# Kernel optimization log

Measured on AMD Instinct MI355X. Metric: run time of the kernel, lower is better.

The kernel has to match this reference:

```python
import jax, jax.numpy as jnp
import numpy as np


def setup_inputs() -> dict:
    key = jax.random.key(0)
    k1, k2, k3, k4 = jax.random.split(key, 4)
    B, T, C, H = 16, 2048, 384, 64
    x = jax.random.normal(k1, (B, T, C), dtype=jnp.float32)
    Wq = jax.random.normal(k2, (C, H), dtype=jnp.float32) * (1.0 / np.sqrt(C))
    Wk = jax.random.normal(k3, (C, H), dtype=jnp.float32) * (1.0 / np.sqrt(C))
    Wv = jax.random.normal(k4, (C, H), dtype=jnp.float32) * (1.0 / np.sqrt(C))
    return {"x": x, "Wq": Wq, "Wk": Wk, "Wv": Wv}


def reference(x, Wq, Wk, Wv):
    # x: [B, T, C]; Wq/Wk/Wv: [C, H]
    T = x.shape[1]
    H = Wk.shape[1]
    q = jnp.einsum('btc,ch->bth', x, Wq)
    k = jnp.einsum('btc,ch->bth', x, Wk)
    v = jnp.einsum('btc,ch->bth', x, Wv)
    scale = 1.0 / jnp.sqrt(jnp.asarray(H, dtype=x.dtype))
    wei = jnp.einsum('bth,bsh->bts', q, k) * scale  # [B, T, T]
    causal = jnp.tril(jnp.ones((T, T), dtype=bool))
    wei = jnp.where(causal, wei, -jnp.inf)
    attn = jax.nn.softmax(wei, axis=-1)
    # dropout p=0 -> identity
    out = jnp.einsum('bts,bsh->bth', attn, v)  # [B, T, H]
    return out
```

## Files before the change

kernel.cpp:

```cpp
#include <hip/hip_runtime.h>
#include <hip/hip_bf16.h>

#define B_ 16
#define T_ 2048
#define C_ 384
#define H_ 64

typedef __attribute__((ext_vector_type(8))) short short8;
typedef __attribute__((ext_vector_type(4))) short short4_t;
typedef __attribute__((ext_vector_type(4))) float floatx4;
typedef __attribute__((ext_vector_type(2))) unsigned int uint2_t;
typedef __attribute__((ext_vector_type(4))) unsigned int uintx4;

#if defined(__has_builtin)
#if __has_builtin(__builtin_amdgcn_mfma_f32_16x16x16bf16_1k)
#define HAVE_MFMA16 1
#endif
#endif

static __device__ __forceinline__ short f2bf(float f) {
    unsigned u = __builtin_bit_cast(unsigned, f);
    u += 0x7FFF + ((u >> 16) & 1);
    return (short)(u >> 16);
}
static __device__ __forceinline__ float bf2f(short s) {
    return __builtin_bit_cast(float, ((unsigned)(unsigned short)s) << 16);
}
static __device__ __forceinline__ unsigned cvt_pk_bf16(float lo, float hi) {
    unsigned r;
    asm("v_cvt_pk_bf16_f32 %0, %1, %2" : "=v"(r) : "v"(lo), "v"(hi));
    return r;
}

__global__ void wt_kernel(const float* __restrict__ Wq, const float* __restrict__ Wk,
                          const float* __restrict__ Wv, short* __restrict__ wt2) {
    int idx = blockIdx.x * 256 + threadIdx.x;
    if (idx >= 12 * 12 * 512) return;
    int f = idx >> 9, within = idx & 511;
    int lane = within >> 3, jj = within & 7;
    int nt16 = f / 12, kc32 = f - nt16 * 12;
    int mat = nt16 >> 2, w = nt16 & 3;
    int quad = lane >> 4, l16 = lane & 15;
    int h = w * 16 + l16;
    int c = kc32 * 32 + quad * 8 + jj;
    const float* W = (mat == 0) ? Wq : ((mat == 1) ? Wk : Wv);
    wt2[idx] = f2bf(W[c * H_ + h]);
}

__global__ __launch_bounds__(256) void qkv_kernel(
        const float* __restrict__ x, const short* __restrict__ wt2,
        short* __restrict__ qo, short* __restrict__ ko, short* __restrict__ vto) {
    __shared__ short xs[32 * 392];

    int b = blockIdx.y, t0 = blockIdx.x * 32;
    int tid = threadIdx.x;

    const float* src = x + (size_t)(b * T_ + t0) * C_;
    for (int i = 0; i < 12; i++) {
        int chunk = i * 256 + tid;
        int row = chunk / 96, off = (chunk % 96) * 4;
        float4 f = *(const float4*)&src[row * 384 + off];
        uint2_t u2;
        u2.x = cvt_pk_bf16(f.x, f.y);
        u2.y = cvt_pk_bf16(f.z, f.w);
        *(uint2_t*)&xs[row * 392 + off] = u2;
    }
    __syncthreads();

    int w = tid >> 6, lane = tid & 63, quad = lane >> 4, l16 = lane & 15;

    floatx4 acc[2][3];
    for (int mt = 0; mt < 2; mt++)
        for (int j = 0; j < 3; j++) acc[mt][j] = (floatx4)0.0f;

    for (int kc = 0; kc < 384; kc += 32) {
        int kc32 = kc >> 5;
        short8 a0 = *(const short8*)&xs[l16 * 392 + kc + quad * 8];
        short8 a1 = *(const short8*)&xs[(16 + l16) * 392 + kc + quad * 8];
        for (int j = 0; j < 3; j++) {
            short8 bf = *(const short8*)&wt2[(((j * 4 + w) * 12) + kc32) * 512 + lane * 8];
            acc[0][j] = __builtin_amdgcn_mfma_f32_16x16x32_bf16(a0, bf, acc[0][j], 0, 0, 0);
            acc[1][j] = __builtin_amdgcn_mfma_f32_16x16x32_bf16(a1, bf, acc[1][j], 0, 0, 0);
        }
    }
    __syncthreads();

    {
        int h = w * 16 + l16;
        for (int j = 0; j < 3; j++)
            for (int mt = 0; mt < 2; mt++)
                for (int r = 0; r < 4; r += 2) {
                    unsigned pk2 = cvt_pk_bf16(acc[mt][j][r], acc[mt][j][r + 1]);
                    int tl0 = mt * 16 + quad * 4 + r;
                    if (j == 0) {
                        xs[tl0 * 72 + h] = (short)pk2;
                        xs[(tl0 + 1) * 72 + h] = (short)(pk2 >> 16);
                    } else if (j == 1) {
                        xs[2304 + tl0 * 72 + h] = (short)pk2;
                        xs[2304 + (tl0 + 1) * 72 + h] = (short)(pk2 >> 16);
                    } else {
                        *(unsigned*)&xs[4608 + h * 40 + tl0] = pk2;
                    }
                }
    }
    __syncthreads();

    {
        int row = tid >> 3, off = (tid & 7) * 8;
        *(short8*)&qo[(size_t)(b * T_ + t0 + row) * H_ + off] = *(const short8*)&xs[row * 72 + off];
        *(short8*)&ko[(size_t)(b * T_ + t0 + row) * H_ + off] = *(const short8*)&xs[2304 + row * 72 + off];
    }
    {
        int h = tid >> 2, off = (tid & 3) * 8;
        *(short8*)&vto[(size_t)(b * H_ + h) * T_ + t0 + off] = *(const short8*)&xs[4608 + h * 40 + off];
    }
}

#define KVSZ (64 * 72)
#define SLOT_BYTES (16384 + 512)

__global__ __launch_bounds__(256) void attn_seg_kernel(
        const short* __restrict__ q, const short* __restrict__ k,
        const short* __restrict__ vt, float* __restrict__ slots) {
    __shared__ short ks[2 * KVSZ];
    __shared__ short vs[2 * KVSZ];
#if !defined(HAVE_MFMA16)
    __shared__ short ps[4 * 16 * 72];
#endif

    int b = blockIdx.y, fid = blockIdx.x, nslot = gridDim.x;
    int tt = 0, cum = 0;
    while (cum + ((2 * tt + 5) >> 2) <= fid) { cum += (2 * tt + 5) >> 2; tt++; }
    int nk = 2 * tt + 2;
    int k0 = (fid - cum) * 4;
    int k1 = min(k0 + 4, nk);

    int tid = threadIdx.x, w = tid >> 6, lane = tid & 63, quad = lane >> 4, l16 = lane & 15;
    int trow0 = tt * 128 + w * 32;

    short8 aq[2][2];
    for (int mt = 0; mt < 2; mt++) {
        const short* qrow = q + (size_t)(b * T_ + trow0 + mt * 16 + l16) * H_;
        aq[mt][0] = *(const short8*)&qrow[quad * 8];
        aq[mt][1] = *(const short8*)&qrow[32 + quad * 8];
    }

    floatx4 o[2][4];
    for (int mt = 0; mt < 2; mt++)
        for (int i = 0; i < 4; i++) o[mt][i] = (floatx4)0.0f;
    float lp[2] = {0.f, 0.f};

    const short* kb0 = k + (size_t)b * T_ * H_;
    const short* vtb = vt + (size_t)b * H_ * T_;

    int srow = tid >> 3, soff = (tid & 7) * 8;
    const float C1 = 0.125f * 1.44269504f;
    const float C2 = 12.0f * 1.44269504f;

    {
        const short* kg = kb0 + (size_t)k0 * 64 * H_;
        const short* vg = vtb + k0 * 64;
        *(short8*)&ks[srow * 72 + soff] = *(const short8*)&kg[srow * H_ + soff];
        *(short8*)&ks[(srow + 32) * 72 + soff] = *(const short8*)&kg[(srow + 32) * H_ + soff];
        *(short8*)&vs[srow * 72 + soff] = *(const short8*)&vg[(size_t)srow * T_ + soff];
        *(short8*)&vs[(srow + 32) * 72 + soff] = *(const short8*)&vg[(size_t)(srow + 32) * T_ + soff];
    }
    __syncthreads();

    int p = 0;
    for (int st = k0; st < k1; st++) {
        bool more = (st + 1 < k1);
        short8 pk0, pk1, pv0, pv1;
        if (more) {
            const short* kg = kb0 + (size_t)(st + 1) * 64 * H_;
            const short* vg = vtb + (st + 1) * 64;
            pk0 = *(const short8*)&kg[srow * H_ + soff];
            pk1 = *(const short8*)&kg[(srow + 32) * H_ + soff];
            pv0 = *(const short8*)&vg[(size_t)srow * T_ + soff];
            pv1 = *(const short8*)&vg[(size_t)(srow + 32) * T_ + soff];
        }
        const short* ksp = ks + p * KVSZ;
        const short* vsp = vs + p * KVSZ;
        int s0 = st * 64;

        floatx4 sacc[2][4];
        for (int mt = 0; mt < 2; mt++)
            for (int nt = 0; nt < 4; nt++) sacc[mt][nt] = (floatx4)0.0f;
        for (int nt = 0; nt < 4; nt++) {
            short8 bk0 = *(const short8*)&ksp[(nt * 16 + l16) * 72 + quad * 8];
            short8 bk1 = *(const short8*)&ksp[(nt * 16 + l16) * 72 + 32 + quad * 8];
            sacc[0][nt] = __builtin_amdgcn_mfma_f32_16x16x32_bf16(bk0, aq[0][0], sacc[0][nt], 0, 0, 0);
            sacc[0][nt] = __builtin_amdgcn_mfma_f32_16x16x32_bf16(bk1, aq[0][1], sacc[0][nt], 0, 0, 0);
            sacc[1][nt] = __builtin_amdgcn_mfma_f32_16x16x32_bf16(bk0, aq[1][0], sacc[1][nt], 0, 0, 0);
            sacc[1][nt] = __builtin_amdgcn_mfma_f32_16x16x32_bf16(bk1, aq[1][1], sacc[1][nt], 0, 0, 0);
        }

        bool diag = (st >= 2 * tt);
#if defined(HAVE_MFMA16)
        short4_t pa[2][4];
        for (int mt = 0; mt < 2; mt++) {
            int q_idx = trow0 + mt * 16 + l16;
            for (int nt = 0; nt < 4; nt++) {
                float pv[4];
                for (int r = 0; r < 4; r++) {
                    float pe = __builtin_amdgcn_exp2f(fmaf(sacc[mt][nt][r], C1, -C2));
                    int s_idx = s0 + nt * 16 + quad * 4 + r;
                    if (diag && (s_idx > q_idx)) pe = 0.0f;
                    lp[mt] += pe;
                    pv[r] = pe;
                }
                uint2_t u;
                u.x = cvt_pk_bf16(pv[0], pv[1]);
                u.y = cvt_pk_bf16(pv[2], pv[3]);
                pa[mt][nt] = __builtin_bit_cast(short4_t, u);
            }
        }
        for (int nh = 0; nh < 4; nh++) {
            const short* vrow = &vsp[(nh * 16 + l16) * 72 + quad * 4];
            for (int c = 0; c < 4; c++) {
                short4_t bv = *(const short4_t*)&vrow[c * 16];
                o[0][nh] = __builtin_amdgcn_mfma_f32_16x16x16bf16_1k(pa[0][c], bv, o[0][nh], 0, 0, 0);
                o[1][nh] = __builtin_amdgcn_mfma_f32_16x16x16bf16_1k(pa[1][c], bv, o[1][nh], 0, 0, 0);
            }
        }
#else
        short* psw = ps + w * 16 * 72;
        short8 ap[2][2];
        for (int mt = 0; mt < 2; mt++) {
            int q_idx = trow0 + mt * 16 + l16;
            for (int nt = 0; nt < 4; nt++)
                for (int r = 0; r < 4; r++) {
                    float pv = __builtin_amdgcn_exp2f(fmaf(sacc[mt][nt][r], C1, -C2));
                    int s_idx = s0 + nt * 16 + quad * 4 + r;
                    if (diag && (s_idx > q_idx)) pv = 0.0f;
                    lp[mt] += pv;
                    psw[l16 * 72 + nt * 16 + quad * 4 + r] = f2bf(pv);
                }
            ap[mt][0] = *(const short8*)&psw[l16 * 72 + quad * 8];
            ap[mt][1] = *(const short8*)&psw[l16 * 72 + 32 + quad * 8];
        }
        for (int nh = 0; nh < 4; nh++) {
            short8 bv0 = *(const short8*)&vsp[(nh * 16 + l16) * 72 + quad * 8];
            short8 bv1 = *(const short8*)&vsp[(nh * 16 + l16) * 72 + 32 + quad * 8];
            o[0][nh] = __builtin_amdgcn_mfma_f32_16x16x32_bf16(ap[0][0], bv0, o[0][nh], 0, 0, 0);
            o[0][nh] = __builtin_amdgcn_mfma_f32_16x16x32_bf16(ap[0][1], bv1, o[0][nh], 0, 0, 0);
            o[1][nh] = __builtin_amdgcn_mfma_f32_16x16x32_bf16(ap[1][0], bv0, o[1][nh], 0, 0, 0);
            o[1][nh] = __builtin_amdgcn_mfma_f32_16x16x32_bf16(ap[1][1], bv1, o[1][nh], 0, 0, 0);
        }
#endif

        if (more) {
            short* kd = ks + (1 - p) * KVSZ;
            short* vd = vs + (1 - p) * KVSZ;
            *(short8*)&kd[srow * 72 + soff] = pk0;
            *(short8*)&kd[(srow + 32) * 72 + soff] = pk1;
            *(short8*)&vd[srow * 72 + soff] = pv0;
            *(short8*)&vd[(srow + 32) * 72 + soff] = pv1;
            __syncthreads();
            p ^= 1;
        }
    }

    for (int mt = 0; mt < 2; mt++) {
        lp[mt] += __shfl_xor(lp[mt], 16);
        lp[mt] += __shfl_xor(lp[mt], 32);
    }

    char* slotb = (char*)slots + ((size_t)b * nslot + fid) * SLOT_BYTES;
    short* slotO = (short*)slotb;
    float* slotL = (float*)(slotb + 16384);

    for (int mt = 0; mt < 2; mt++)
        for (int nh = 0; nh < 4; nh++)
            for (int r = 0; r < 4; r += 2) {
                unsigned pk2 = cvt_pk_bf16(o[mt][nh][r], o[mt][nh][r + 1]);
                slotO[(w * 32 + mt * 16 + quad * 4 + r) * 64 + nh * 16 + l16] = (short)pk2;
                slotO[(w * 32 + mt * 16 + quad * 4 + r + 1) * 64 + nh * 16 + l16] = (short)(pk2 >> 16);
            }
    if (quad == 0)
        for (int mt = 0; mt < 2; mt++)
            slotL[w * 32 + mt * 16 + l16] = lp[mt];
}

__global__ __launch_bounds__(256) void combine_kernel(
        const float* __restrict__ slots, int nslot, float* __restrict__ out) {
    int b = blockIdx.y, tb = blockIdx.x;
    int tt = tb >> 1;
    int nseg = (2 * tt + 5) >> 2;
    int cum = 0;
    for (int i = 0; i < tt; i++) cum += (2 * i + 5) >> 2;
    const char* base = (const char*)slots + ((size_t)b * nslot + cum) * SLOT_BYTES;

    int tid = threadIdx.x;
    int row = (tb & 1) * 64 + (tid >> 2);
    int qo = (tid & 3) * 16;
    float acc[16];
    for (int i = 0; i < 16; i++) acc[i] = 0.f;
    float lsum = 0.f;
    for (int s = 0; s < nseg; s++) {
        const short* O = (const short*)(base + (size_t)s * SLOT_BYTES);
        const float* L = (const float*)(base + (size_t)s * SLOT_BYTES + 16384);
        for (int i = 0; i < 2; i++) {
            short8 v = *(const short8*)&O[row * 64 + qo + i * 8];
            uintx4 u = __builtin_bit_cast(uintx4, v);
            for (int j = 0; j < 4; j++) {
                acc[i * 8 + 2 * j]     += __builtin_bit_cast(float, u[j] << 16);
                acc[i * 8 + 2 * j + 1] += __builtin_bit_cast(float, u[j] & 0xFFFF0000u);
            }
        }
        lsum += L[row];
    }
    float inv = 1.0f / lsum;
    float* op = out + (size_t)(b * T_ + tt * 128 + row) * H_ + qo;
    for (int i = 0; i < 4; i++) {
        float4 v;
        v.x = acc[i * 4 + 0] * inv; v.y = acc[i * 4 + 1] * inv;
        v.z = acc[i * 4 + 2] * inv; v.w = acc[i * 4 + 3] * inv;
        *(float4*)&op[i * 4] = v;
    }
}

template<bool DIAG>
static __device__ __forceinline__ void attn_step(
        int s0, int t0w, int quad, int l16,
        const short* __restrict__ kbase, const short* __restrict__ vtb,
        short8 aq0, short8 aq1, short* __restrict__ psw,
        floatx4 (&o)[4], float (&lpart)[4]) {
    floatx4 sacc[4];
    for (int nt = 0; nt < 4; nt++) sacc[nt] = (floatx4)0.0f;
    for (int nt = 0; nt < 4; nt++) {
        short8 bk0 = *(const short8*)&kbase[(nt * 16 + l16) * H_ + quad * 8];
        short8 bk1 = *(const short8*)&kbase[(nt * 16 + l16) * H_ + 32 + quad * 8];
        sacc[nt] = __builtin_amdgcn_mfma_f32_16x16x32_bf16(aq0, bk0, sacc[nt], 0, 0, 0);
        sacc[nt] = __builtin_amdgcn_mfma_f32_16x16x32_bf16(aq1, bk1, sacc[nt], 0, 0, 0);
    }
    const float C1 = 0.125f * 1.44269504f;
    const float C2 = 12.0f * 1.44269504f;
    for (int nt = 0; nt < 4; nt++) {
        int s_idx = s0 + nt * 16 + l16;
        for (int r = 0; r < 4; r++) {
            float p = __builtin_amdgcn_exp2f(fmaf(sacc[nt][r], C1, -C2));
            if (DIAG && (s_idx > t0w + quad * 4 + r)) p = 0.0f;
            lpart[r] += p;
            psw[(quad * 4 + r) * 72 + nt * 16 + l16] = f2bf(p);
        }
    }
    short8 ap0 = *(const short8*)&psw[l16 * 72 + quad * 8];
    short8 ap1 = *(const short8*)&psw[l16 * 72 + 32 + quad * 8];
    for (int nh = 0; nh < 4; nh++) {
        short8 bv0 = *(const short8*)&vtb[(size_t)(nh * 16 + l16) * T_ + s0 + quad * 8];
        short8 bv1 = *(const short8*)&vtb[(size_t)(nh * 16 + l16) * T_ + s0 + 32 + quad * 8];
        o[nh] = __builtin_amdgcn_mfma_f32_16x16x32_bf16(ap0, bv0, o[nh], 0, 0, 0);
        o[nh] = __builtin_amdgcn_mfma_f32_16x16x32_bf16(ap1, bv1, o[nh], 0, 0, 0);
    }
}

__global__ __launch_bounds__(256) void attn_kernel(
        const short* __restrict__ q, const short* __restrict__ k,
        const short* __restrict__ vt, float* __restrict__ out) {
    __shared__ short ps[4 * 16 * 72];

    int b = blockIdx.y;
    int g = ((int)blockIdx.x + 4 * (b & 7)) & 31;
    int tt = (b < 8) ? g : 31 - g;
    int t0 = tt * 64;
    int tid = threadIdx.x, w = tid >> 6, lane = tid & 63, quad = lane >> 4, l16 = lane & 15;
    int t0w = t0 + w * 16;

    const short* qrow = q + (size_t)(b * T_ + t0w + l16) * H_;
    short8 aq0 = *(const short8*)&qrow[quad * 8];
    short8 aq1 = *(const short8*)&qrow[32 + quad * 8];

    floatx4 o[4];
    for (int nh = 0; nh < 4; nh++) o[nh] = (floatx4)0.0f;
    float lpart[4] = {0.f, 0.f, 0.f, 0.f};

    const short* kb0 = k + (size_t)b * T_ * H_;
    const short* vtb = vt + (size_t)b * H_ * T_;
    short* psw = ps + w * 16 * 72;

    for (int st = 0; st < tt; st++)
        attn_step<false>(st * 64, t0w, quad, l16, kb0 + (size_t)st * 64 * H_,
                         vtb, aq0, aq1, psw, o, lpart);
    attn_step<true>(tt * 64, t0w, quad, l16, kb0 + (size_t)tt * 64 * H_,
                    vtb, aq0, aq1, psw, o, lpart);

    for (int d = 1; d < 16; d <<= 1)
        for (int r = 0; r < 4; r++)
            lpart[r] += __shfl_xor(lpart[r], d, 16);

    for (int nh = 0; nh < 4; nh++)
        for (int r = 0; r < 4; r++) {
            int t = t0w + quad * 4 + r;
            out[(size_t)(b * T_ + t) * H_ + nh * 16 + l16] = o[nh][r] / lpart[r];
        }
}

extern "C" void kernel_launch(void* const* d_in, const int* in_sizes, int n_in,
                              void* d_out, int out_size, void* d_ws, size_t ws_size,
                              hipStream_t stream) {
    const float* x  = (const float*)d_in[0];
    const float* Wq = (const float*)d_in[1];
    const float* Wk = (const float*)d_in[2];
    const float* Wv = (const float*)d_in[3];

    char* ws = (char*)d_ws;
    short* qb  = (short*)(ws);
    short* kb  = (short*)(ws + (size_t)4 * 1024 * 1024);
    short* vtb = (short*)(ws + (size_t)8 * 1024 * 1024);
    short* wtb = (short*)(ws + (size_t)12 * 1024 * 1024);
    float* slots = (float*)(ws + (size_t)12 * 1024 * 1024 + 256 * 1024);
    size_t base_need = (size_t)12 * 1024 * 1024 + 256 * 1024;

    wt_kernel<<<dim3(288), dim3(256), 0, stream>>>(Wq, Wk, Wv, wtb);
    qkv_kernel<<<dim3(T_ / 32, B_), dim3(256), 0, stream>>>(x, wtb, qb, kb, vtb);

    float* out = (float*)d_out;
    const int NSLOT = 72;
    if (ws_size >= base_need + (size_t)B_ * NSLOT * (size_t)SLOT_BYTES) {
        attn_seg_kernel<<<dim3(NSLOT, B_), dim3(256), 0, stream>>>(qb, kb, vtb, slots);
        combine_kernel<<<dim3(T_ / 64, B_), dim3(256), 0, stream>>>(slots, NSLOT, out);
    } else {
        attn_kernel<<<dim3(T_ / 64, B_), dim3(256), 0, stream>>>(qb, kb, vtb, out);
    }
}
```

Measured before the change: 133.8 us.

## Enlarge QKV tile to 64 rows, add MFMA priority hints, split causal masking path

```diff
diff --git a/kernel.cpp b/kernel.cpp
--- a/kernel.cpp
+++ b/kernel.cpp
@@ -50,13 +50,13 @@
 __global__ __launch_bounds__(256) void qkv_kernel(
         const float* __restrict__ x, const short* __restrict__ wt2,
         short* __restrict__ qo, short* __restrict__ ko, short* __restrict__ vto) {
-    __shared__ short xs[32 * 392];
-
-    int b = blockIdx.y, t0 = blockIdx.x * 32;
+    __shared__ short xs[64 * 392];
+
+    int b = blockIdx.y, t0 = blockIdx.x * 64;
     int tid = threadIdx.x;
 
     const float* src = x + (size_t)(b * T_ + t0) * C_;
-    for (int i = 0; i < 12; i++) {
+    for (int i = 0; i < 24; i++) {
         int chunk = i * 256 + tid;
         int row = chunk / 96, off = (chunk % 96) * 4;
         float4 f = *(const float4*)&src[row * 384 + off];
@@ -69,18 +69,19 @@
 
     int w = tid >> 6, lane = tid & 63, quad = lane >> 4, l16 = lane & 15;
 
-    floatx4 acc[2][3];
-    for (int mt = 0; mt < 2; mt++)
+    floatx4 acc[4][3];
+    for (int mt = 0; mt < 4; mt++)
         for (int j = 0; j < 3; j++) acc[mt][j] = (floatx4)0.0f;
 
     for (int kc = 0; kc < 384; kc += 32) {
         int kc32 = kc >> 5;
-        short8 a0 = *(const short8*)&xs[l16 * 392 + kc + quad * 8];
-        short8 a1 = *(const short8*)&xs[(16 + l16) * 392 + kc + quad * 8];
+        short8 a[4];
+        for (int mt = 0; mt < 4; mt++)
+            a[mt] = *(const short8*)&xs[(mt * 16 + l16) * 392 + kc + quad * 8];
         for (int j = 0; j < 3; j++) {
             short8 bf = *(const short8*)&wt2[(((j * 4 + w) * 12) + kc32) * 512 + lane * 8];
-            acc[0][j] = __builtin_amdgcn_mfma_f32_16x16x32_bf16(a0, bf, acc[0][j], 0, 0, 0);
-            acc[1][j] = __builtin_amdgcn_mfma_f32_16x16x32_bf16(a1, bf, acc[1][j], 0, 0, 0);
+            for (int mt = 0; mt < 4; mt++)
+                acc[mt][j] = __builtin_amdgcn_mfma_f32_16x16x32_bf16(a[mt], bf, acc[mt][j], 0, 0, 0);
         }
     }
     __syncthreads();
@@ -88,7 +89,7 @@
     {
         int h = w * 16 + l16;
         for (int j = 0; j < 3; j++)
-            for (int mt = 0; mt < 2; mt++)
+            for (int mt = 0; mt < 4; mt++)
                 for (int r = 0; r < 4; r += 2) {
                     unsigned pk2 = cvt_pk_bf16(acc[mt][j][r], acc[mt][j][r + 1]);
                     int tl0 = mt * 16 + quad * 4 + r;
@@ -96,10 +97,10 @@
                         xs[tl0 * 72 + h] = (short)pk2;
                         xs[(tl0 + 1) * 72 + h] = (short)(pk2 >> 16);
                     } else if (j == 1) {
-                        xs[2304 + tl0 * 72 + h] = (short)pk2;
-                        xs[2304 + (tl0 + 1) * 72 + h] = (short)(pk2 >> 16);
+                        xs[4608 + tl0 * 72 + h] = (short)pk2;
+                        xs[4608 + (tl0 + 1) * 72 + h] = (short)(pk2 >> 16);
                     } else {
-                        *(unsigned*)&xs[4608 + h * 40 + tl0] = pk2;
+                        *(unsigned*)&xs[9216 + h * 72 + tl0] = pk2;
                     }
                 }
     }
@@ -107,12 +108,16 @@
 
     {
         int row = tid >> 3, off = (tid & 7) * 8;
-        *(short8*)&qo[(size_t)(b * T_ + t0 + row) * H_ + off] = *(const short8*)&xs[row * 72 + off];
-        *(short8*)&ko[(size_t)(b * T_ + t0 + row) * H_ + off] = *(const short8*)&xs[2304 + row * 72 + off];
+        for (int i = 0; i < 2; i++) {
+            int rr = row + i * 32;
+            *(short8*)&qo[(size_t)(b * T_ + t0 + rr) * H_ + off] = *(const short8*)&xs[rr * 72 + off];
+            *(short8*)&ko[(size_t)(b * T_ + t0 + rr) * H_ + off] = *(const short8*)&xs[4608 + rr * 72 + off];
+        }
     }
     {
-        int h = tid >> 2, off = (tid & 3) * 8;
-        *(short8*)&vto[(size_t)(b * H_ + h) * T_ + t0 + off] = *(const short8*)&xs[4608 + h * 40 + off];
+        int h = tid >> 2, off = (tid & 3) * 16;
+        *(short8*)&vto[(size_t)(b * H_ + h) * T_ + t0 + off] = *(const short8*)&xs[9216 + h * 72 + off];
+        *(short8*)&vto[(size_t)(b * H_ + h) * T_ + t0 + off + 8] = *(const short8*)&xs[9216 + h * 72 + off + 8];
     }
 }
 
@@ -186,6 +191,7 @@
         floatx4 sacc[2][4];
         for (int mt = 0; mt < 2; mt++)
             for (int nt = 0; nt < 4; nt++) sacc[mt][nt] = (floatx4)0.0f;
+        __builtin_amdgcn_s_setprio(1);
         for (int nt = 0; nt < 4; nt++) {
             short8 bk0 = *(const short8*)&ksp[(nt * 16 + l16) * 72 + quad * 8];
             short8 bk1 = *(const short8*)&ksp[(nt * 16 + l16) * 72 + 32 + quad * 8];
@@ -194,27 +200,47 @@
             sacc[1][nt] = __builtin_amdgcn_mfma_f32_16x16x32_bf16(bk0, aq[1][0], sacc[1][nt], 0, 0, 0);
             sacc[1][nt] = __builtin_amdgcn_mfma_f32_16x16x32_bf16(bk1, aq[1][1], sacc[1][nt], 0, 0, 0);
         }
+        __builtin_amdgcn_s_setprio(0);
 
         bool diag = (st >= 2 * tt);
 #if defined(HAVE_MFMA16)
         short4_t pa[2][4];
-        for (int mt = 0; mt < 2; mt++) {
-            int q_idx = trow0 + mt * 16 + l16;
-            for (int nt = 0; nt < 4; nt++) {
-                float pv[4];
-                for (int r = 0; r < 4; r++) {
-                    float pe = __builtin_amdgcn_exp2f(fmaf(sacc[mt][nt][r], C1, -C2));
-                    int s_idx = s0 + nt * 16 + quad * 4 + r;
-                    if (diag && (s_idx > q_idx)) pe = 0.0f;
-                    lp[mt] += pe;
-                    pv[r] = pe;
+        if (!diag) {
+            for (int mt = 0; mt < 2; mt++) {
+                float ts[4];
+                for (int nt = 0; nt < 4; nt++) {
+                    float pv[4];
+                    for (int r = 0; r < 4; r++)
+                        pv[r] = __builtin_amdgcn_exp2f(fmaf(sacc[mt][nt][r], C1, -C2));
+                    uint2_t u;
+                    u.x = cvt_pk_bf16(pv[0], pv[1]);
+                    u.y = cvt_pk_bf16(pv[2], pv[3]);
+                    pa[mt][nt] = __builtin_bit_cast(short4_t, u);
+                    ts[nt] = (pv[0] + pv[1]) + (pv[2] + pv[3]);
                 }
-                uint2_t u;
-                u.x = cvt_pk_bf16(pv[0], pv[1]);
-                u.y = cvt_pk_bf16(pv[2], pv[3]);
-                pa[mt][nt] = __builtin_bit_cast(short4_t, u);
+                lp[mt] += (ts[0] + ts[1]) + (ts[2] + ts[3]);
             }
-        }
+        } else {
+            for (int mt = 0; mt < 2; mt++) {
+                int q_idx = trow0 + mt * 16 + l16;
+                float ts[4];
+                for (int nt = 0; nt < 4; nt++) {
+                    float pv[4];
+                    for (int r = 0; r < 4; r++) {
+                        float pe = __builtin_amdgcn_exp2f(fmaf(sacc[mt][nt][r], C1, -C2));
+                        int s_idx = s0 + nt * 16 + quad * 4 + r;
+                        pv[r] = (s_idx > q_idx) ? 0.0f : pe;
+                    }
+                    uint2_t u;
+                    u.x = cvt_pk_bf16(pv[0], pv[1]);
+                    u.y = cvt_pk_bf16(pv[2], pv[3]);
+                    pa[mt][nt] = __builtin_bit_cast(short4_t, u);
+                    ts[nt] = (pv[0] + pv[1]) + (pv[2] + pv[3]);
+                }
+                lp[mt] += (ts[0] + ts[1]) + (ts[2] + ts[3]);
+            }
+        }
+        __builtin_amdgcn_s_setprio(1);
         for (int nh = 0; nh < 4; nh++) {
             const short* vrow = &vsp[(nh * 16 + l16) * 72 + quad * 4];
             for (int c = 0; c < 4; c++) {
@@ -223,6 +249,7 @@
                 o[1][nh] = __builtin_amdgcn_mfma_f32_16x16x16bf16_1k(pa[1][c], bv, o[1][nh], 0, 0, 0);
             }
         }
+        __builtin_amdgcn_s_setprio(0);
 #else
         short* psw = ps + w * 16 * 72;
         short8 ap[2][2];
@@ -413,7 +440,7 @@
     size_t base_need = (size_t)12 * 1024 * 1024 + 256 * 1024;
 
     wt_kernel<<<dim3(288), dim3(256), 0, stream>>>(Wq, Wk, Wv, wtb);
-    qkv_kernel<<<dim3(T_ / 32, B_), dim3(256), 0, stream>>>(x, wtb, qb, kb, vtb);
+    qkv_kernel<<<dim3(T_ / 64, B_), dim3(256), 0, stream>>>(x, wtb, qb, kb, vtb);
 
     float* out = (float*)d_out;
     const int NSLOT = 72;
```

Result: faster. 129.9 us (-2.9%).
